# Kernel tuning notes

Measured on AMD Instinct MI355X. Metric: run time of the kernel, lower is better.

Reference implementation:

```python
import jax, jax.numpy as jnp
import numpy as np

HIDDEN = 1024
NUM_HEAD = 16
HEAD_DIM = HIDDEN // NUM_HEAD


def setup_inputs() -> dict:
    key = jax.random.key(0)
    ks = jax.random.split(key, 9)
    B, S = 1, 4096
    scale = 1.0 / np.sqrt(HIDDEN)
    inp = {
        "x": jax.random.normal(ks[0], (B, S, HIDDEN), dtype=jnp.float32),
        "wq": jax.random.normal(ks[1], (HIDDEN, HIDDEN), dtype=jnp.float32) * scale,
        "bq": jnp.zeros((HIDDEN,), dtype=jnp.float32),
        "wk": jax.random.normal(ks[2], (HIDDEN, HIDDEN), dtype=jnp.float32) * scale,
        "bk": jnp.zeros((HIDDEN,), dtype=jnp.float32),
        "wv": jax.random.normal(ks[3], (HIDDEN, HIDDEN), dtype=jnp.float32) * scale,
        "bv": jnp.zeros((HIDDEN,), dtype=jnp.float32),
        "wo": jax.random.normal(ks[4], (HIDDEN, HIDDEN), dtype=jnp.float32) * scale,
        "bo": jnp.zeros((HIDDEN,), dtype=jnp.float32),
    }
    return inp


def reference(x, wq, bq, wk, bk, wv, bv, wo, bo):
    B, S, _ = x.shape
    # QKV projections (torch Linear: x @ W.T + b)
    def split_heads(t):
        return t.reshape(B, S, NUM_HEAD, HEAD_DIM).transpose(0, 2, 1, 3)  # [B,H,S,D]
    q = split_heads(x @ wq.T + bq)
    k = split_heads(x @ wk.T + bk)
    v = split_heads(x @ wv.T + bv)
    # scaled dot-product scores: [B,H,S,S]
    scores = jnp.einsum('bhsd,bhtd->bhst', q, k) / jnp.sqrt(jnp.float32(HEAD_DIM))
    # faithful double softmax over the key axis (no mask; dropout = eval identity)
    attn = jax.nn.softmax(scores, axis=-1)
    attn = jax.nn.softmax(attn, axis=-1)
    out = jnp.einsum('bhst,bhtd->bhsd', attn, v)  # [B,H,S,D]
    out = out.transpose(0, 2, 1, 3).reshape(B, S, HIDDEN)
    return out @ wo.T + bo
```

## Files before the change

### kernel.cpp

```cpp
#include <hip/hip_runtime.h>
#include <hip/hip_bf16.h>
#include <stdint.h>

#define S 4096
#define HID 1024
#define NH 16
#define DH 64

typedef __attribute__((ext_vector_type(8))) short short8;
typedef __attribute__((ext_vector_type(2))) float f32x2;
typedef __attribute__((ext_vector_type(4))) float f32x4;
typedef __attribute__((ext_vector_type(16))) float f32x16;
typedef __attribute__((ext_vector_type(4))) unsigned int u32x4;

#define VMCNT8 asm volatile("s_waitcnt vmcnt(8)" ::: "memory")
#define VMCNT0 asm volatile("s_waitcnt vmcnt(0)" ::: "memory")
#define LGKM0  asm volatile("s_waitcnt lgkmcnt(0)" ::: "memory")

__device__ __forceinline__ unsigned short f2bf(float f) {
  unsigned int u = __builtin_bit_cast(unsigned int, f);
  u += 0x7FFF + ((u >> 16) & 1);
  return (unsigned short)(u >> 16);
}
__device__ __forceinline__ unsigned int pktrunc(float lo, float hi) {
  return __builtin_amdgcn_perm(__builtin_bit_cast(unsigned int, hi),
                               __builtin_bit_cast(unsigned int, lo), 0x07060302u);
}
__device__ __forceinline__ void gload16(const unsigned short* g, unsigned short* l) {
  __builtin_amdgcn_global_load_lds((const __attribute__((address_space(1))) unsigned int*)g,
                                   (__attribute__((address_space(3))) unsigned int*)l, 16, 0, 0);
}

__global__ __launch_bounds__(256) void cast_kernel(
    const float* __restrict__ x,  const float* __restrict__ wq,
    const float* __restrict__ wk, const float* __restrict__ wv,
    const float* __restrict__ wo,
    unsigned short* __restrict__ xb,  unsigned short* __restrict__ wqb,
    unsigned short* __restrict__ wkb, unsigned short* __restrict__ wvb,
    unsigned short* __restrict__ wob, float* __restrict__ vsum)
{
  const int y = blockIdx.y, bx = blockIdx.x;
  const float* src; unsigned short* dst; int cx;
  if (y < 4)       { src = x;  dst = xb;  cx = y * 1024 + bx; }
  else if (y == 4) { src = wq; dst = wqb; cx = bx; }
  else if (y == 5) { src = wk; dst = wkb; cx = bx; }
  else if (y == 6) { src = wv; dst = wvb; cx = bx; }
  else             { src = wo; dst = wob; cx = bx; }
  if (y == 4 && bx == 0) {
    f32x4 z = {0.f, 0.f, 0.f, 0.f};
    reinterpret_cast<f32x4*>(vsum)[threadIdx.x] = z;
  }
  int i = (cx * 256 + threadIdx.x) * 4;
  float4 v = *reinterpret_cast<const float4*>(src + i);
  ushort4 o;
  o.x = f2bf(v.x); o.y = f2bf(v.y); o.z = f2bf(v.z); o.w = f2bf(v.w);
  *reinterpret_cast<ushort4*>(dst + i) = o;
}

__device__ __forceinline__ void gemm128(
    const unsigned short* __restrict__ A, const unsigned short* __restrict__ W,
    unsigned short* As, unsigned short* Bs, f32x4 acc[4][4], int row0, int col0)
{
  const int tid = threadIdx.x;
  const int wave = tid >> 6, lane = tid & 63, quad = lane >> 4, l16 = lane & 15;
  const int wr = (wave >> 1) * 64, wc = (wave & 1) * 64;
  const int srow = lane >> 2, sseg = lane & 3;
  const f32x4 z = {0.f, 0.f, 0.f, 0.f};
  #pragma unroll
  for (int i = 0; i < 4; i++)
    #pragma unroll
    for (int j = 0; j < 4; j++) acc[i][j] = z;

  for (int k0 = 0; k0 < HID; k0 += 32) {
    __syncthreads();
    #pragma unroll
    for (int c = 0; c < 2; c++) {
      const int rbase = c * 64 + wave * 16;
      gload16(A + (size_t)(row0 + rbase + srow) * HID + k0 + sseg * 8, As + rbase * 32);
      gload16(W + (size_t)(col0 + rbase + srow) * HID + k0 + sseg * 8, Bs + rbase * 32);
    }
    __syncthreads();

    short8 af[4], bfr[4];
    #pragma unroll
    for (int i = 0; i < 4; i++)
      af[i] = *reinterpret_cast<const short8*>(As + (wr + i * 16 + l16) * 32 + quad * 8);
    #pragma unroll
    for (int j = 0; j < 4; j++)
      bfr[j] = *reinterpret_cast<const short8*>(Bs + (wc + j * 16 + l16) * 32 + quad * 8);
    #pragma unroll
    for (int i = 0; i < 4; i++)
      #pragma unroll
      for (int j = 0; j < 4; j++)
        acc[i][j] = __builtin_amdgcn_mfma_f32_16x16x32_bf16(af[i], bfr[j], acc[i][j], 0, 0, 0);
  }
}

__global__ __launch_bounds__(256) void qkv_gemm_kernel(
    const unsigned short* __restrict__ X,
    const unsigned short* __restrict__ Wq, const unsigned short* __restrict__ Wk,
    const unsigned short* __restrict__ Wv,
    const float* __restrict__ bq, const float* __restrict__ bk, const float* __restrict__ bv,
    unsigned short* __restrict__ Qo, unsigned short* __restrict__ K2o, unsigned short* __restrict__ Vbo,
    float* __restrict__ Vsum)
{
  __shared__ unsigned short As[128 * 32];
  __shared__ unsigned short Bs[128 * 32];
  __shared__ unsigned short Ep[16384];
  const int zsel = blockIdx.z;
  const unsigned short* W = (zsel == 0) ? Wq : (zsel == 1) ? Wk : Wv;
  const float* bias        = (zsel == 0) ? bq : (zsel == 1) ? bk : bv;
  const int row0 = blockIdx.x * 128, col0 = blockIdx.y * 128;
  f32x4 acc[4][4];
  gemm128(X, W, As, Bs, acc, row0, col0);

  const int tid = threadIdx.x;
  const int wave = tid >> 6, lane = tid & 63, quad = lane >> 4, l16 = lane & 15;
  const int wr = (wave >> 1) * 64, wc = (wave & 1) * 64;
  const int h0 = col0 >> 6, g0 = row0 >> 5;

  if (zsel == 0) {
    const float osc = 0.18033688011112042f;
    #pragma unroll
    for (int j = 0; j < 4; j++) {
      int rc = wc + j * 16 + l16;
      float bb = bias[col0 + rc];
      int hh = rc >> 6, d = rc & 63;
      #pragma unroll
      for (int i = 0; i < 4; i++)
        #pragma unroll
        for (int rr = 0; rr < 4; rr++) {
          int srel = wr + i * 16 + quad * 4 + rr;
          Ep[hh * 8192 + srel * 64 + d] = f2bf((acc[i][j][rr] + bb) * osc);
        }
    }
  } else if (zsel == 1) {
    #pragma unroll
    for (int j = 0; j < 4; j++) {
      int rc = wc + j * 16 + l16;
      float bb = bias[col0 + rc];
      int hh = rc >> 6, dh = rc & 63;
      int c = dh >> 4, hfk = (dh >> 3) & 1, j8 = dh & 7;
      #pragma unroll
      for (int i = 0; i < 4; i++)
        #pragma unroll
        for (int rr = 0; rr < 4; rr++) {
          int srel = wr + i * 16 + quad * 4 + rr;
          int gl = srel >> 5, l32k = srel & 31;
          Ep[(hh * 4 + gl) * 2048 + (c * 64 + hfk * 32 + l32k) * 8 + j8] =
              f2bf(acc[i][j][rr] + bb);
        }
    }
  } else {
    #pragma unroll
    for (int j = 0; j < 4; j++) {
      int rc = wc + j * 16 + l16;
      float bb = bias[col0 + rc];
      int hh = rc >> 6, dh = rc & 63;
      int ng = dh >> 5, l32v = dh & 31;
      int hf_v = quad & 1, jj0 = (quad >> 1) * 4;
      float colsum = 0.f;
      #pragma unroll
      for (int i = 0; i < 4; i++) {
        int gt4 = (wr + i * 16) >> 5;
        int grp = i & 1;
        float v0 = acc[i][j][0] + bb, v1 = acc[i][j][1] + bb;
        float v2 = acc[i][j][2] + bb, v3 = acc[i][j][3] + bb;
        colsum += (v0 + v1) + (v2 + v3);
        ushort4 pv;
        pv.x = f2bf(v0); pv.y = f2bf(v1); pv.z = f2bf(v2); pv.w = f2bf(v3);
        *reinterpret_cast<ushort4*>(
            Ep + (((hh * 4 + gt4) * 2 + grp) * 2 + ng) * 512 + (hf_v * 32 + l32v) * 8 + jj0) = pv;
      }
      colsum += __shfl_xor(colsum, 16);
      colsum += __shfl_xor(colsum, 32);
      if (quad == 0) atomicAdd(&Vsum[col0 + rc], colsum);
    }
  }
  __syncthreads();

  #pragma unroll
  for (int it = 0; it < 8; it++) {
    int flat = it * 2048 + tid * 8;
    u32x4 v = *reinterpret_cast<const u32x4*>(Ep + flat);
    if (zsel == 0) {
      int hh = flat >> 13;
      size_t goff = ((size_t)(h0 + hh) * S + row0) * 64 + (flat & 8191);
      *reinterpret_cast<u32x4*>(Qo + goff) = v;
    } else if (zsel == 1) {
      int sp = flat >> 11, hh = sp >> 2, g4 = sp & 3;
      size_t goff = (size_t)((h0 + hh) * 128 + g0 + g4) * 2048 + (flat & 2047);
      *reinterpret_cast<u32x4*>(K2o + goff) = v;
    } else {
      int sp = flat >> 9;
      int ng = sp & 1, grp = (sp >> 1) & 1, gt4 = (sp >> 2) & 3, hh = sp >> 4;
      size_t goff = (size_t)((((h0 + hh) * 128 + g0 + gt4) * 2 + grp) * 2 + ng) * 512 + (flat & 511);
      *reinterpret_cast<u32x4*>(Vbo + goff) = v;
    }
  }
}

__global__ __launch_bounds__(256) void out_gemm_kernel(
    const unsigned short* __restrict__ A, const unsigned short* __restrict__ W,
    const float* __restrict__ be, float* __restrict__ dst)
{
  __shared__ unsigned short As[128 * 32];
  __shared__ unsigned short Bs[128 * 32];
  const int row0 = blockIdx.x * 128, col0 = blockIdx.y * 128;
  f32x4 acc[4][4];
  gemm128(A, W, As, Bs, acc, row0, col0);

  const int tid = threadIdx.x;
  const int wave = tid >> 6, lane = tid & 63, quad = lane >> 4, l16 = lane & 15;
  const int wr = (wave >> 1) * 64, wc = (wave & 1) * 64;
  #pragma unroll
  for (int j = 0; j < 4; j++) {
    int n = col0 + wc + j * 16 + l16;
    float bb = be[n];
    #pragma unroll
    for (int i = 0; i < 4; i++)
      #pragma unroll
      for (int rr = 0; rr < 4; rr++) {
        int s = row0 + wr + i * 16 + quad * 4 + rr;
        dst[(size_t)s * HID + n] = acc[i][j][rr] + bb;
      }
  }
}

struct AttnState {
  short8 qf[2][4];
  f32x16 Oa[2][2];
  f32x16 zacc;
  f32x2  zp[2];
};

__device__ __forceinline__ void loadregs(
    const unsigned short* kb, const unsigned short* vb,
    short8 (&kf)[4], short8 (&vf)[4])
{
  #pragma unroll
  for (int c = 0; c < 4; c++)
    kf[c] = *reinterpret_cast<const short8*>(kb + c * 512);
  #pragma unroll
  for (int w = 0; w < 4; w++)
    vf[w] = *reinterpret_cast<const short8*>(vb + w * 512);
}

__device__ __forceinline__ void attn_compute(
    const short8 (&kf)[4], const short8 (&vfr)[4], AttnState& st)
{
  #pragma unroll
  for (int qh = 0; qh < 2; qh++) {
    f32x16 acc = __builtin_amdgcn_mfma_f32_32x32x16_bf16(kf[0], st.qf[qh][0], st.zacc, 0, 0, 0);
    #pragma unroll
    for (int c = 1; c < 4; c++)
      acc = __builtin_amdgcn_mfma_f32_32x32x16_bf16(kf[c], st.qf[qh][c], acc, 0, 0, 0);

    unsigned int D[8];
    #pragma unroll
    for (int m = 0; m < 8; m++) {
      float t0 = __builtin_amdgcn_exp2f(acc[2 * m]);
      float t1 = __builtin_amdgcn_exp2f(acc[2 * m + 1]);
      f32x2 t = {t0, t1};
      st.zp[qh] += t;
      D[m] = pktrunc(t0, t1);
    }
    u32x4 dv0 = {D[0], D[1], D[2], D[3]};
    u32x4 dv1 = {D[4], D[5], D[6], D[7]};
    short8 A0 = __builtin_bit_cast(short8, dv0);
    short8 A1 = __builtin_bit_cast(short8, dv1);

    st.Oa[qh][0] = __builtin_amdgcn_mfma_f32_32x32x16_bf16(A0, vfr[0], st.Oa[qh][0], 0, 0, 0);
    st.Oa[qh][1] = __builtin_amdgcn_mfma_f32_32x32x16_bf16(A0, vfr[1], st.Oa[qh][1], 0, 0, 0);
    st.Oa[qh][0] = __builtin_amdgcn_mfma_f32_32x32x16_bf16(A1, vfr[2], st.Oa[qh][0], 0, 0, 0);
    st.Oa[qh][1] = __builtin_amdgcn_mfma_f32_32x32x16_bf16(A1, vfr[3], st.Oa[qh][1], 0, 0, 0);
  }
}

__device__ __forceinline__ void stage_tile(
    const unsigned short* gK, const unsigned short* gV,
    unsigned short* lK, unsigned short* lV)
{
  #pragma unroll
  for (int i = 0; i < 4; i++) gload16(gK + i * 512, lK + i * 512);
  #pragma unroll
  for (int i = 0; i < 4; i++) gload16(gV + i * 512, lV + i * 512);
}

__global__ __launch_bounds__(256, 2) void attn_kernel(
    const unsigned short* __restrict__ Q, const unsigned short* __restrict__ K2,
    const unsigned short* __restrict__ Vb, unsigned short* __restrict__ OUT,
    const float* __restrict__ Vsum, const float* __restrict__ wo,
    const float* __restrict__ bo, float* __restrict__ be)
{
  if (blockIdx.y == 16) {
    const int base = blockIdx.x * 16 + (threadIdx.x >> 6) * 4;
    const int l = threadIdx.x & 63;
    #pragma unroll
    for (int c = 0; c < 4; c++) {
      const int n = base + c;
      float acc = 0.f;
      #pragma unroll
      for (int i = 0; i < 16; i++)
        acc += Vsum[l + 64 * i] * wo[(size_t)n * HID + l + 64 * i];
      #pragma unroll
      for (int off = 32; off >= 1; off >>= 1) acc += __shfl_xor(acc, off);
      if (l == 0) be[n] = bo[n] + acc * (1.f / 4097.f);
    }
    return;
  }

  __shared__ unsigned short T[4][2][2][2048];
  __shared__ float Zl[256];
  float* Ored = reinterpret_cast<float*>(&T[0][0][0][0]);

  const int lin = blockIdx.y * 64 + blockIdx.x;
  const int xcd = lin & 7, idx = lin >> 3;
  const int h = xcd * 2 + (idx >> 6);
  const int q0 = (idx & 63) * 64;

  const int tid = threadIdx.x;
  const int wave = tid >> 6, lane = tid & 63, hf = lane >> 5, l32 = lane & 31;

  AttnState st;
  #pragma unroll
  for (int qh = 0; qh < 2; qh++) {
    const unsigned short* qrow = Q + (size_t)(h * S + q0 + qh * 32 + l32) * DH;
    #pragma unroll
    for (int c = 0; c < 4; c++)
      st.qf[qh][c] = *reinterpret_cast<const short8*>(qrow + c * 16 + hf * 8);
  }
  #pragma unroll
  for (int r = 0; r < 16; r++) {
    st.zacc[r] = 0.f;
    st.Oa[0][0][r] = 0.f; st.Oa[0][1][r] = 0.f;
    st.Oa[1][0][r] = 0.f; st.Oa[1][1][r] = 0.f;
  }
  st.zp[0] = (f32x2){0.f, 0.f};
  st.zp[1] = (f32x2){0.f, 0.f};

  const unsigned short* Kb  = K2 + (size_t)h * 128 * 2048;
  const unsigned short* Vbb = Vb + (size_t)h * 128 * 2048;

  const unsigned short* gK = Kb  + (size_t)wave * 2048 + (size_t)lane * 8;
  const unsigned short* gV = Vbb + (size_t)wave * 2048 + (size_t)lane * 8;
  unsigned short* lK0 = &T[wave][0][0][0];
  unsigned short* lV0 = &T[wave][0][1][0];
  unsigned short* lK1 = &T[wave][1][0][0];
  unsigned short* lV1 = &T[wave][1][1][0];
  const unsigned short* kb0 = &T[wave][0][0][0] + lane * 8;
  const unsigned short* vb0 = &T[wave][0][1][0] + lane * 8;
  const unsigned short* kb1 = &T[wave][1][0][0] + lane * 8;
  const unsigned short* vb1 = &T[wave][1][1][0] + lane * 8;
  const ptrdiff_t STR = 4 * 2048;

  short8 kA[4], vA[4], kB[4], vB[4];

  stage_tile(gK, gV, lK0, lV0); gK += STR; gV += STR;
  VMCNT0;
  loadregs(kb0, vb0, kA, vA);
  stage_tile(gK, gV, lK1, lV1); gK += STR; gV += STR;
  LGKM0;

  for (int p = 0; p < 15; p++) {
    stage_tile(gK, gV, lK0, lV0); gK += STR; gV += STR;
    VMCNT8;
    loadregs(kb1, vb1, kB, vB);
    attn_compute(kA, vA, st);
    LGKM0;
    stage_tile(gK, gV, lK1, lV1); gK += STR; gV += STR;
    VMCNT8;
    loadregs(kb0, vb0, kA, vA);
    attn_compute(kB, vB, st);
    LGKM0;
  }
  VMCNT0;
  loadregs(kb1, vb1, kB, vB);
  attn_compute(kA, vA, st);
  attn_compute(kB, vB, st);

  __syncthreads();
  {
    float za = st.zp[0][0] + st.zp[0][1];
    float zb = st.zp[1][0] + st.zp[1][1];
    za += __shfl_xor(za, 32);
    zb += __shfl_xor(zb, 32);
    if (hf == 0) {
      Zl[wave * 64 + l32]      = za;
      Zl[wave * 64 + 32 + l32] = zb;
    }
    float* Ow = Ored + wave * 4096;
    #pragma unroll
    for (int qh = 0; qh < 2; qh++)
      #pragma unroll
      for (int ng = 0; ng < 2; ng++)
        #pragma unroll
        for (int r = 0; r < 16; r++) {
          const int row = (r & 3) + 8 * (r >> 2) + 4 * hf;
          Ow[(qh * 32 + row) * 64 + ng * 32 + l32] = st.Oa[qh][ng][r];
        }
  }
  __syncthreads();
  {
    const int q = tid >> 2, d0 = (tid & 3) * 16;
    const float* O0 = Ored + q * 64 + d0;
    f32x4 s0 = *reinterpret_cast<const f32x4*>(O0);
    f32x4 s1 = *reinterpret_cast<const f32x4*>(O0 + 4);
    f32x4 s2 = *reinterpret_cast<const f32x4*>(O0 + 8);
    f32x4 s3 = *reinterpret_cast<const f32x4*>(O0 + 12);
    #pragma unroll
    for (int w = 1; w < 4; w++) {
      const float* Ow = Ored + w * 4096 + q * 64 + d0;
      s0 += *reinterpret_cast<const f32x4*>(Ow);
      s1 += *reinterpret_cast<const f32x4*>(Ow + 4);
      s2 += *reinterpret_cast<const f32x4*>(Ow + 8);
      s3 += *reinterpret_cast<const f32x4*>(Ow + 12);
    }
    const float zt = Zl[q] + Zl[64 + q] + Zl[128 + q] + Zl[192 + q];
    const float rz = 1.f / (zt * 4097.f);
    unsigned short* op = OUT + (size_t)(q0 + q) * HID + h * DH + d0;
    ushort4 u;
    u.x = f2bf(s0[0] * rz); u.y = f2bf(s0[1] * rz);
    u.z = f2bf(s0[2] * rz); u.w = f2bf(s0[3] * rz);
    *reinterpret_cast<ushort4*>(op) = u;
    u.x = f2bf(s1[0] * rz); u.y = f2bf(s1[1] * rz);
    u.z = f2bf(s1[2] * rz); u.w = f2bf(s1[3] * rz);
    *reinterpret_cast<ushort4*>(op + 4) = u;
    u.x = f2bf(s2[0] * rz); u.y = f2bf(s2[1] * rz);
    u.z = f2bf(s2[2] * rz); u.w = f2bf(s2[3] * rz);
    *reinterpret_cast<ushort4*>(op + 8) = u;
    u.x = f2bf(s3[0] * rz); u.y = f2bf(s3[1] * rz);
    u.z = f2bf(s3[2] * rz); u.w = f2bf(s3[3] * rz);
    *reinterpret_cast<ushort4*>(op + 12) = u;
  }
}

extern "C" void kernel_launch(void* const* d_in, const int* in_sizes, int n_in,
                              void* d_out, int out_size, void* d_ws, size_t ws_size,
                              hipStream_t stream) {
  const float* x  = (const float*)d_in[0];
  const float* wq = (const float*)d_in[1];
  const float* bq = (const float*)d_in[2];
  const float* wk = (const float*)d_in[3];
  const float* bk = (const float*)d_in[4];
  const float* wv = (const float*)d_in[5];
  const float* bv = (const float*)d_in[6];
  const float* wo = (const float*)d_in[7];
  const float* bo = (const float*)d_in[8];
  float* out = (float*)d_out;

  char* ws = (char*)d_ws;
  unsigned short* xb  = (unsigned short*)(ws);
  unsigned short* wqb = (unsigned short*)(ws + (8u  << 20));
  unsigned short* wkb = (unsigned short*)(ws + (10u << 20));
  unsigned short* wvb = (unsigned short*)(ws + (12u << 20));
  unsigned short* wob = (unsigned short*)(ws + (14u << 20));
  unsigned short* qw  = (unsigned short*)(ws + (16u << 20));
  unsigned short* k2  = (unsigned short*)(ws + (24u << 20));
  unsigned short* vb  = (unsigned short*)(ws + (32u << 20));
  float* vsum         = (float*)(ws + (40u << 20));
  float* be           = (float*)(ws + (40u << 20) + 65536);
  unsigned short* aw  = xb;

  cast_kernel<<<dim3(1024, 8), 256, 0, stream>>>(x, wq, wk, wv, wo, xb, wqb, wkb, wvb, wob, vsum);
  qkv_gemm_kernel<<<dim3(32, 8, 3), 256, 0, stream>>>(xb, wqb, wkb, wvb, bq, bk, bv, qw, k2, vb, vsum);
  attn_kernel<<<dim3(64, 17), 256, 0, stream>>>(qw, k2, vb, aw, vsum, wo, bo, be);
  out_gemm_kernel<<<dim3(32, 8, 1), 256, 0, stream>>>(aw, wob, be, out);
}
```

Before: 235.5 us.

## Load V fragments directly from global, halve LDS, raise occupancy to three blocks

V tiles are now read straight from global memory into registers instead of being staged through LDS, so the LDS buffer shrinks to K only (32KB instead of 64KB). Launch bounds rise to three blocks per CU to use the freed LDS. The cross-wave O reduction is reworked into two phases so it fits in the smaller buffer: waves 2-3 write, then waves 0-1 accumulate in place. The trade-off is a tighter register budget at the higher occupancy and global-load latency for V, which the wait counts now have to cover.

```diff
diff --git a/kernel.cpp b/kernel.cpp
--- a/kernel.cpp
+++ b/kernel.cpp
@@ -14,6 +14,7 @@
 typedef __attribute__((ext_vector_type(4))) unsigned int u32x4;
 
 #define VMCNT8 asm volatile("s_waitcnt vmcnt(8)" ::: "memory")
+#define VMCNT4 asm volatile("s_waitcnt vmcnt(4)" ::: "memory")
 #define VMCNT0 asm volatile("s_waitcnt vmcnt(0)" ::: "memory")
 #define LGKM0  asm volatile("s_waitcnt lgkmcnt(0)" ::: "memory")
 
@@ -234,16 +235,20 @@
   f32x2  zp[2];
 };
 
-__device__ __forceinline__ void loadregs(
-    const unsigned short* kb, const unsigned short* vb,
-    short8 (&kf)[4], short8 (&vf)[4])
+__device__ __forceinline__ void loadK(
+    const unsigned short* kb, short8 (&kf)[4])
 {
   #pragma unroll
   for (int c = 0; c < 4; c++)
     kf[c] = *reinterpret_cast<const short8*>(kb + c * 512);
+}
+
+__device__ __forceinline__ void loadV(
+    const unsigned short* gVt, short8 (&vf)[4])
+{
   #pragma unroll
   for (int w = 0; w < 4; w++)
-    vf[w] = *reinterpret_cast<const short8*>(vb + w * 512);
+    vf[w] = *reinterpret_cast<const short8*>(gVt + w * 512);
 }
 
 __device__ __forceinline__ void attn_compute(
@@ -277,17 +282,14 @@
   }
 }
 
-__device__ __forceinline__ void stage_tile(
-    const unsigned short* gK, const unsigned short* gV,
-    unsigned short* lK, unsigned short* lV)
+__device__ __forceinline__ void stageK(
+    const unsigned short* gK, unsigned short* lK)
 {
   #pragma unroll
   for (int i = 0; i < 4; i++) gload16(gK + i * 512, lK + i * 512);
-  #pragma unroll
-  for (int i = 0; i < 4; i++) gload16(gV + i * 512, lV + i * 512);
-}
-
-__global__ __launch_bounds__(256, 2) void attn_kernel(
+}
+
+__global__ __launch_bounds__(256, 3) void attn_kernel(
     const unsigned short* __restrict__ Q, const unsigned short* __restrict__ K2,
     const unsigned short* __restrict__ Vb, unsigned short* __restrict__ OUT,
     const float* __restrict__ Vsum, const float* __restrict__ wo,
@@ -310,9 +312,9 @@
     return;
   }
 
-  __shared__ unsigned short T[4][2][2][2048];
+  __shared__ unsigned short T[4][2][2048];
   __shared__ float Zl[256];
-  float* Ored = reinterpret_cast<float*>(&T[0][0][0][0]);
+  float* Ored = reinterpret_cast<float*>(&T[0][0][0]);
 
   const int lin = blockIdx.y * 64 + blockIdx.x;
   const int xcd = lin & 7, idx = lin >> 3;
@@ -342,41 +344,46 @@
   const unsigned short* Kb  = K2 + (size_t)h * 128 * 2048;
   const unsigned short* Vbb = Vb + (size_t)h * 128 * 2048;
 
-  const unsigned short* gK = Kb  + (size_t)wave * 2048 + (size_t)lane * 8;
-  const unsigned short* gV = Vbb + (size_t)wave * 2048 + (size_t)lane * 8;
-  unsigned short* lK0 = &T[wave][0][0][0];
-  unsigned short* lV0 = &T[wave][0][1][0];
-  unsigned short* lK1 = &T[wave][1][0][0];
-  unsigned short* lV1 = &T[wave][1][1][0];
-  const unsigned short* kb0 = &T[wave][0][0][0] + lane * 8;
-  const unsigned short* vb0 = &T[wave][0][1][0] + lane * 8;
-  const unsigned short* kb1 = &T[wave][1][0][0] + lane * 8;
-  const unsigned short* vb1 = &T[wave][1][1][0] + lane * 8;
+  const unsigned short* gKb = Kb  + (size_t)wave * 2048 + (size_t)lane * 8;
+  const unsigned short* gVb = Vbb + (size_t)wave * 2048 + (size_t)lane * 8;
+  unsigned short* lK0 = &T[wave][0][0];
+  unsigned short* lK1 = &T[wave][1][0];
+  const unsigned short* kb0 = &T[wave][0][0] + lane * 8;
+  const unsigned short* kb1 = &T[wave][1][0] + lane * 8;
   const ptrdiff_t STR = 4 * 2048;
 
   short8 kA[4], vA[4], kB[4], vB[4];
 
-  stage_tile(gK, gV, lK0, lV0); gK += STR; gV += STR;
-  VMCNT0;
-  loadregs(kb0, vb0, kA, vA);
-  stage_tile(gK, gV, lK1, lV1); gK += STR; gV += STR;
+  stageK(gKb, lK0);
+  loadV(gVb, vA);
+  stageK(gKb + STR, lK1);
+  VMCNT4;
+  loadK(kb0, kA);
   LGKM0;
 
+  const unsigned short* gK2 = gKb + 2 * STR;
+  const unsigned short* gV1 = gVb + STR;
+
   for (int p = 0; p < 15; p++) {
-    stage_tile(gK, gV, lK0, lV0); gK += STR; gV += STR;
+    stageK(gK2, lK0); gK2 += STR;
+    loadV(gV1, vB);   gV1 += STR;
     VMCNT8;
-    loadregs(kb1, vb1, kB, vB);
+    loadK(kb1, kB);
     attn_compute(kA, vA, st);
     LGKM0;
-    stage_tile(gK, gV, lK1, lV1); gK += STR; gV += STR;
+    stageK(gK2, lK1); gK2 += STR;
+    loadV(gV1, vA);   gV1 += STR;
     VMCNT8;
-    loadregs(kb0, vb0, kA, vA);
+    loadK(kb0, kA);
     attn_compute(kB, vB, st);
     LGKM0;
   }
+  loadV(gV1, vB);
+  VMCNT4;
+  loadK(kb1, kB);
+  attn_compute(kA, vA, st);
+  LGKM0;
   VMCNT0;
-  loadregs(kb1, vb1, kB, vB);
-  attn_compute(kA, vA, st);
   attn_compute(kB, vB, st);
 
   __syncthreads();
@@ -389,6 +396,21 @@
       Zl[wave * 64 + l32]      = za;
       Zl[wave * 64 + 32 + l32] = zb;
     }
+    if (wave >= 2) {
+      float* Ow = Ored + (wave - 2) * 4096;
+      #pragma unroll
+      for (int qh = 0; qh < 2; qh++)
+        #pragma unroll
+        for (int ng = 0; ng < 2; ng++)
+          #pragma unroll
+          for (int r = 0; r < 16; r++) {
+            const int row = (r & 3) + 8 * (r >> 2) + 4 * hf;
+            Ow[(qh * 32 + row) * 64 + ng * 32 + l32] = st.Oa[qh][ng][r];
+          }
+    }
+  }
+  __syncthreads();
+  if (wave < 2) {
     float* Ow = Ored + wave * 4096;
     #pragma unroll
     for (int qh = 0; qh < 2; qh++)
@@ -397,25 +419,19 @@
         #pragma unroll
         for (int r = 0; r < 16; r++) {
           const int row = (r & 3) + 8 * (r >> 2) + 4 * hf;
-          Ow[(qh * 32 + row) * 64 + ng * 32 + l32] = st.Oa[qh][ng][r];
+          const int ix = (qh * 32 + row) * 64 + ng * 32 + l32;
+          Ow[ix] += st.Oa[qh][ng][r];
         }
   }
   __syncthreads();
   {
     const int q = tid >> 2, d0 = (tid & 3) * 16;
     const float* O0 = Ored + q * 64 + d0;
-    f32x4 s0 = *reinterpret_cast<const f32x4*>(O0);
-    f32x4 s1 = *reinterpret_cast<const f32x4*>(O0 + 4);
-    f32x4 s2 = *reinterpret_cast<const f32x4*>(O0 + 8);
-    f32x4 s3 = *reinterpret_cast<const f32x4*>(O0 + 12);
-    #pragma unroll
-    for (int w = 1; w < 4; w++) {
-      const float* Ow = Ored + w * 4096 + q * 64 + d0;
-      s0 += *reinterpret_cast<const f32x4*>(Ow);
-      s1 += *reinterpret_cast<const f32x4*>(Ow + 4);
-      s2 += *reinterpret_cast<const f32x4*>(Ow + 8);
-      s3 += *reinterpret_cast<const f32x4*>(Ow + 12);
-    }
+    const float* O1 = Ored + 4096 + q * 64 + d0;
+    f32x4 s0 = *reinterpret_cast<const f32x4*>(O0)      + *reinterpret_cast<const f32x4*>(O1);
+    f32x4 s1 = *reinterpret_cast<const f32x4*>(O0 + 4)  + *reinterpret_cast<const f32x4*>(O1 + 4);
+    f32x4 s2 = *reinterpret_cast<const f32x4*>(O0 + 8)  + *reinterpret_cast<const f32x4*>(O1 + 8);
+    f32x4 s3 = *reinterpret_cast<const f32x4*>(O0 + 12) + *reinterpret_cast<const f32x4*>(O1 + 12);
     const float zt = Zl[q] + Zl[64 + q] + Zl[128 + q] + Zl[192 + q];
     const float rz = 1.f / (zt * 4097.f);
     unsigned short* op = OUT + (size_t)(q0 + q) * HID + h * DH + d0;
```

After: 380.6 us. 61.6% more time.
